# Kernel optimization log

Measured on AMD Instinct MI355X. Metric: run time of the kernel, lower is better.

## Reference

```python
import jax, jax.numpy as jnp
import numpy as np

B, N, K, G = 8, 2048, 20, 8
EPS = 1e-5

def lrelu(v):
    return jnp.where(v >= 0, v, 0.2 * v)

def group_norm(x, gamma, beta):
    # x: (B, C, ...); normalize over channel groups and spatial dims
    b, c = x.shape[0], x.shape[1]
    xg = x.reshape(b, G, c // G, -1)
    mu = xg.mean(axis=(2, 3), keepdims=True)
    var = xg.var(axis=(2, 3), keepdims=True)
    xn = ((xg - mu) * jax.lax.rsqrt(var + EPS)).reshape(x.shape)
    sh = (1, c) + (1,) * (x.ndim - 2)
    return xn * gamma.reshape(sh) + beta.reshape(sh)

def graph_feature(x, k):
    # x: (B, C, N) -> edge features (B, 2C, N, k)
    inner = 2.0 * jnp.einsum('bcn,bcm->bnm', x, x)
    xx = jnp.sum(x * x, axis=1)                     # (B, N)
    pd = -(xx[:, :, None] - inner + xx[:, None, :]) # negative squared dist
    idx = jax.lax.top_k(pd, k)[1]                   # (B, N, k) nearest
    xt = jnp.swapaxes(x, 1, 2)                      # (B, N, C)
    nbr = jax.vmap(lambda f, i: f[i])(xt, idx)      # (B, N, k, C) gather
    ctr = jnp.broadcast_to(xt[:, :, None, :], nbr.shape)
    feat = jnp.concatenate([nbr - ctr, ctr], axis=-1)  # (B, N, k, 2C)
    return jnp.transpose(feat, (0, 3, 1, 2))

def edge_block(x, w, b, g, h):
    f = graph_feature(x, K)
    y = jnp.einsum('oc,bcnk->bonk', w, f) + b[None, :, None, None]
    return lrelu(group_norm(y, g, h)).max(axis=-1)   # (B, out, N)

def _forward(x, w0, b0, g0, h0, w1, b1, g1, h1, w2, b2, g2, h2,
             w3, b3, g3, h3, fw0, fb0, fw1, fb1, fw2, fb2):
    cur = jnp.swapaxes(x, 1, 2)                      # (B, 3, N)
    res = []
    for (w, b, g, h) in ((w0, b0, g0, h0), (w1, b1, g1, h1), (w2, b2, g2, h2)):
        cur = edge_block(cur, w, b, g, h)
        res.append(cur)
    xc = jnp.concatenate(res, axis=1)                # (B, 256, N)
    pf = jnp.einsum('oc,bcn->bon', w3, xc) + b3[None, :, None]
    pf = lrelu(group_norm(pf, g3, h3))               # (B, 256, N)
    v = jnp.concatenate([pf.max(axis=-1), pf.mean(axis=-1)], axis=1)  # (B, 512)
    v = lrelu(v @ fw0.T + fb0)
    v = lrelu(v @ fw1.T + fb1)
    return v @ fw2.T + fb2                           # (B, 256)

def setup_inputs():
    key = jax.random.key(0)
    ks = jax.random.split(key, 16)
    def rn(k, shape, s=0.05):
        return jax.random.normal(k, shape, jnp.float32) * s
    inp = {'x': jax.random.normal(ks[0], (B, N, 3), jnp.float32)}
    inp.update(w0=rn(ks[1], (64, 6)), b0=rn(ks[2], (64,)), g0=jnp.ones((64,)), h0=jnp.zeros((64,)))
    inp.update(w1=rn(ks[3], (64, 128)), b1=rn(ks[4], (64,)), g1=jnp.ones((64,)), h1=jnp.zeros((64,)))
    inp.update(w2=rn(ks[5], (128, 128)), b2=rn(ks[6], (128,)), g2=jnp.ones((128,)), h2=jnp.zeros((128,)))
    inp.update(w3=rn(ks[7], (256, 256)), b3=rn(ks[8], (256,)), g3=jnp.ones((256,)), h3=jnp.zeros((256,)))
    inp.update(fw0=rn(ks[9], (512, 512)), fb0=rn(ks[10], (512,)))
    inp.update(fw1=rn(ks[11], (512, 512)), fb1=rn(ks[12], (512,)))
    inp.update(fw2=rn(ks[13], (256, 512)), fb2=rn(ks[14], (256,)))
    return inp

def reference(x, w0, b0, g0, h0, w1, b1, g1, h1, w2, b2, g2, h2,
              w3, b3, g3, h3, fw0, fb0, fw1, fb1, fw2, fb2):
    return _forward(x, w0, b0, g0, h0, w1, b1, g1, h1, w2, b2, g2, h2,
                    w3, b3, g3, h3, fw0, fb0, fw1, fb1, fw2, fb2)
```

## Files before the change

kernel.cpp:

```cpp
#include <hip/hip_runtime.h>
#include <hip/hip_bf16.h>
#include <cstdint>


constexpr int B = 8, N = 2048, KNN = 20, G = 8;
constexpr int BN = B * N;
constexpr float EPS = 1e-5f;

using bf16 = __hip_bfloat16;
using u64 = unsigned long long;

__device__ __forceinline__ float lrelu(float v){ return v >= 0.f ? v : 0.2f * v; }
__device__ __forceinline__ unsigned fenc(float f){ unsigned u = __float_as_uint(f); return (u & 0x80000000u) ? ~u : (u | 0x80000000u); }
__device__ __forceinline__ float fdec(unsigned u){ return (u & 0x80000000u) ? __uint_as_float(u & 0x7FFFFFFFu) : __uint_as_float(~u); }

template<int NB>
__device__ __forceinline__ void batcher_sort(unsigned* s){
  #pragma unroll
  for (int p = 1; p < NB; p <<= 1){
    #pragma unroll
    for (int k = p; k >= 1; k >>= 1){
      #pragma unroll
      for (int j = k % p; j <= NB-1-k; j += 2*k){
        #pragma unroll
        for (int i = 0; i <= ((k-1 < NB-1-j-k) ? k-1 : NB-1-j-k); ++i){
          if ((i + j) / (2*p) == (i + j + k) / (2*p)){
            const unsigned lo = min(s[i+j], s[i+j+k]);
            const unsigned hi = max(s[i+j], s[i+j+k]);
            s[i+j] = lo; s[i+j+k] = hi;
          }
        }
      }
    }
  }
}

template<int NB>
__device__ __forceinline__ void topk_update(unsigned* L, const unsigned* s){
  #pragma unroll
  for (int i = 0; i < NB; ++i) L[i] = min(L[i], s[i]);
  #pragma unroll
  for (int gap = 16; gap >= 1; gap >>= 1){
    #pragma unroll
    for (int i = 0; i < 32; ++i){
      if ((i & ((gap<<1)-1)) < gap){
        const unsigned hi = max(L[i], L[i+gap]);
        const unsigned lo = min(L[i], L[i+gap]);
        L[i] = hi; L[i+gap] = lo;
      }
    }
  }
}

__device__ __forceinline__ u64 knn_dec8(unsigned kk, int q){
  const unsigned ord = kk & 255u;
  const unsigned gidx = (ord >> 4)*128u + (unsigned)q + 8u*(ord & 15u);
  return ((u64)(kk & 0xFFFFFF00u) << 24) | gidx;
}

__device__ __forceinline__ void knn_merge32(unsigned char* ovl, const unsigned* L,
    int* __restrict__ knn_out, size_t bp, int r0, int sr, int sq){
  unsigned* mbuf = (unsigned*)ovl;
  #pragma unroll
  for (int k = 0; k < KNN; ++k) mbuf[(sr*8 + sq)*KNN + k] = L[31-k];
  __syncthreads();
  if (sq == 0){
    int h[8]; u64 v[8];
    #pragma unroll
    for (int q = 0; q < 8; ++q){ h[q] = 0; v[q] = knn_dec8(mbuf[(sr*8+q)*KNN], q); }
    int* outp = &knn_out[(bp + r0 + sr)*KNN];
    for (int k = 0; k < KNN; ++k){
      int best = 0; u64 bv = v[0];
      #pragma unroll
      for (int q = 1; q < 8; ++q) if (v[q] < bv){ bv = v[q]; best = q; }
      outp[k] = (int)(unsigned)(bv & 0xFFFFu);
      #pragma unroll
      for (int q = 0; q < 8; ++q) if (q == best){
        ++h[q];
        v[q] = (h[q] < KNN) ? knn_dec8(mbuf[(sr*8+q)*KNN + h[q]], q) : ~0ULL;
      }
    }
  }
}

struct SrcPtrs { const void* p[23]; };

__global__ __launch_bounds__(256) void convert_kernel(SrcPtrs sp, float* __restrict__ dst,
                                                      float* gstat, unsigned* vmax, float* vmean){
  if (blockIdx.y == 23){
    int t = blockIdx.x * 256 + threadIdx.x;
    if (t < 512) gstat[t] = 0.f;
    if (t < B*256){ vmax[t] = 0x007FFFFFu; vmean[t] = 0.f; }
    return;
  }
  constexpr int CNT[23] = {49152,384,64,64,64,8192,64,64,64,16384,128,128,128,
                           65536,256,256,256,262144,512,262144,512,131072,256};
  constexpr int OFF[23] = {0,49152,49536,49600,49664,49728,57920,57984,58048,58112,
                           74496,74624,74752,74880,140416,140672,140928,141184,
                           403328,403840,665984,666496,797568};
  const int ti = blockIdx.y;
  const int cnt = CNT[ti], off = OFF[ti];
  const unsigned g0w = *(const unsigned*)sp.p[3];
  const bool isbf = (g0w & 0xFFFFu) == 0x3F80u;
  const float* fs = (const float*)sp.p[ti];
  const unsigned short* bs = (const unsigned short*)sp.p[ti];
  for (int j = blockIdx.x*256 + threadIdx.x; j < cnt; j += gridDim.x*256){
    dst[off + j] = isbf ? __uint_as_float((unsigned)bs[j] << 16) : fs[j];
  }
}

template<int C>
__global__ __launch_bounds__(256) void sqnorm_cm(const float* __restrict__ f, float* __restrict__ cn){
  const int p = blockIdx.x*256 + threadIdx.x;
  float s = 0.f;
  #pragma unroll 8
  for (int c = 0; c < C; ++c){ const float v = f[(size_t)c*BN + p]; s += v*v; }
  cn[p] = s;
}

template<int C>
__global__ __launch_bounds__(256) void knn_kernel(const float* __restrict__ feat, const float* __restrict__ cnG,
                                                  int* __restrict__ knn_out){
  constexpr int ROWS = 32, CT = 128, DTP = 133;
  constexpr int COLF_BYTES = C*CT*4;
  __shared__ __align__(16) unsigned char ovl[COLF_BYTES];
  __shared__ __align__(16) float rowfT[C][ROWS];
  float* colfT = (float*)ovl;
  float* dbuf  = (float*)ovl;

  const int t = threadIdx.x;
  const int b = blockIdx.y;
  const int r0 = blockIdx.x * ROWS;
  const size_t bp = (size_t)b * N;
  const int rg = (t & 7)*4;
  const int cg = (t >> 3)*4;
  const int sr = t >> 3;
  const int sq = t & 7;
  const float rn = cnG[bp + r0 + sr];

  for (int i = t; i < C*(ROWS/4); i += 256){
    const int c = i >> 3, r4 = (i & 7)*4;
    *(float4*)&rowfT[c][r4] = *(const float4*)&feat[(size_t)c*BN + bp + r0 + r4];
  }

  unsigned L[32];
  #pragma unroll
  for (int k = 0; k < 32; ++k) L[k] = 0xFFFFFFFFu;

  for (int ct = 0; ct < N/CT; ++ct){
    const int m0 = ct * CT;
    __syncthreads();
    for (int i = t; i < C*(CT/4); i += 256){
      const int c = i >> 5, m4 = (i & 31)*4;
      *(float4*)&colfT[c*CT + m4] = *(const float4*)&feat[(size_t)c*BN + bp + m0 + m4];
    }
    const float4 cn4 = *(const float4*)&cnG[bp + m0 + cg];
    __syncthreads();

    float acc[4][4];
    #pragma unroll
    for (int i=0;i<4;i++){
      #pragma unroll
      for (int j=0;j<4;j++) acc[i][j]=0.f; }
    for (int c = 0; c < C; ++c){
      float4 ar = *(const float4*)&rowfT[c][rg];
      float4 cl = *(const float4*)&colfT[c*CT + cg];
      acc[0][0]+=ar.x*cl.x; acc[0][1]+=ar.x*cl.y; acc[0][2]+=ar.x*cl.z; acc[0][3]+=ar.x*cl.w;
      acc[1][0]+=ar.y*cl.x; acc[1][1]+=ar.y*cl.y; acc[1][2]+=ar.y*cl.z; acc[1][3]+=ar.y*cl.w;
      acc[2][0]+=ar.z*cl.x; acc[2][1]+=ar.z*cl.y; acc[2][2]+=ar.z*cl.z; acc[2][3]+=ar.z*cl.w;
      acc[3][0]+=ar.w*cl.x; acc[3][1]+=ar.w*cl.y; acc[3][2]+=ar.w*cl.z; acc[3][3]+=ar.w*cl.w;
    }
    __syncthreads();
    #pragma unroll
    for (int i=0;i<4;i++){
      float4 s;
      s.x = cn4.x - 2.f*acc[i][0]; s.y = cn4.y - 2.f*acc[i][1];
      s.z = cn4.z - 2.f*acc[i][2]; s.w = cn4.w - 2.f*acc[i][3];
      *(float4*)&dbuf[(rg+i)*DTP + cg] = s;
    }
    __syncthreads();

    const float* drow = &dbuf[sr*DTP];
    unsigned s16[16];
    #pragma unroll
    for (int j = 0; j < 16; ++j){
      const float d = fmaxf(drow[sq + 8*j] + rn, 0.f);
      s16[j] = (__float_as_uint(d) & 0xFFFFFF00u) | (unsigned)(ct*16 + j);
    }
    batcher_sort<16>(s16);
    topk_update<16>(L, s16);
  }

  __syncthreads();
  knn_merge32(ovl, L, knn_out, bp, r0, sr, sq);
}

__global__ __launch_bounds__(256) void knn3_kernel(const float* __restrict__ x, int* __restrict__ knn_out){
  constexpr int ROWS = 32, CT = 128;
  constexpr int MERGE_BYTES = ROWS*8*KNN*4;
  __shared__ __align__(16) unsigned char ovl[MERGE_BYTES];
  float* cx = (float*)ovl;
  float* cy = cx + CT;
  float* cz = cy + CT;

  const int t = threadIdx.x;
  const int b = blockIdx.y;
  const int r0 = blockIdx.x * ROWS;
  const size_t bp = (size_t)b * N;
  const int sr = t >> 3, sq = t & 7;
  const float rx = x[(bp + r0 + sr)*3 + 0];
  const float ry = x[(bp + r0 + sr)*3 + 1];
  const float rz = x[(bp + r0 + sr)*3 + 2];

  unsigned L[32];
  #pragma unroll
  for (int k = 0; k < 32; ++k) L[k] = 0xFFFFFFFFu;

  for (int ct = 0; ct < N/CT; ++ct){
    __syncthreads();
    if (t < CT){
      const size_t q = (bp + ct*CT + t)*3;
      cx[t] = x[q]; cy[t] = x[q+1]; cz[t] = x[q+2];
    }
    __syncthreads();
    unsigned s16[16];
    #pragma unroll
    for (int j = 0; j < 16; ++j){
      const int m = sq + 8*j;
      const float dx = rx - cx[m], dy = ry - cy[m], dz = rz - cz[m];
      const float d = dx*dx + dy*dy + dz*dz;
      s16[j] = (__float_as_uint(d) & 0xFFFFFF00u) | (unsigned)(ct*16 + j);
    }
    batcher_sort<16>(s16);
    topk_update<16>(L, s16);
  }

  __syncthreads();
  knn_merge32(ovl, L, knn_out, bp, r0, sr, sq);
}

template<int C, int COUT, int MT, bool CM>
__global__ __launch_bounds__(256) void zu_kernel(const float* __restrict__ feat, const float* __restrict__ w,
                                                 const float* __restrict__ bias,
                                                 float* __restrict__ z, float* __restrict__ u){
  __shared__ __align__(16) float fT[C][MT+4];
  __shared__ __align__(16) float Wt[C][COUT+4];
  const int t = threadIdx.x;
  const size_t p0 = (size_t)blockIdx.x * MT;
  if constexpr (CM){
    for (int i = t; i < C*(MT/4); i += 256){
      const int c = i / (MT/4), m4 = (i % (MT/4))*4;
      float4 v = *(const float4*)&feat[(size_t)c*BN + p0 + m4];
      *(float4*)&fT[c][m4] = v;
    }
  } else {
    for (int i = t; i < MT*C; i += 256){ int m = i / C, c = i - m*C; fT[c][m] = feat[(p0+m)*C + c]; }
  }
  for (int i = t; i < COUT*C; i += 256){ int o = i / C, c = i - o*C; Wt[c][o] = w[o*(2*C) + c]; }
  __syncthreads();
  constexpr int MQ = MT/4;
  const int rq = t % MQ, oq = t / MQ;
  const int mm = rq*4, oo = oq*8;
  float acc[4][8];
  #pragma unroll
  for (int i=0;i<4;i++){
    #pragma unroll
    for (int j=0;j<8;j++) acc[i][j] = 0.f; }
  for (int c = 0; c < C; ++c){
    float fr[4], wv[8];
    { float4 v = *(const float4*)&fT[c][mm]; fr[0]=v.x; fr[1]=v.y; fr[2]=v.z; fr[3]=v.w; }
    { float4 v = *(const float4*)&Wt[c][oo];   wv[0]=v.x; wv[1]=v.y; wv[2]=v.z; wv[3]=v.w; }
    { float4 v = *(const float4*)&Wt[c][oo+4]; wv[4]=v.x; wv[5]=v.y; wv[6]=v.z; wv[7]=v.w; }
    #pragma unroll
    for (int i=0;i<4;i++){
      #pragma unroll
      for (int j=0;j<8;j++) acc[i][j] += fr[i]*wv[j];
    }
  }
  #pragma unroll
  for (int i=0;i<4;i++){
    float4 s0, s1;
    s0.x=acc[i][0]; s0.y=acc[i][1]; s0.z=acc[i][2]; s0.w=acc[i][3];
    s1.x=acc[i][4]; s1.y=acc[i][5]; s1.z=acc[i][6]; s1.w=acc[i][7];
    *(float4*)&z[(p0+mm+i)*COUT + oo]     = s0;
    *(float4*)&z[(p0+mm+i)*COUT + oo + 4] = s1;
  }
  __syncthreads();
  for (int i = t; i < COUT*C; i += 256){
    int o = i / C, c = i - o*C;
    Wt[c][o] = w[o*2*C + C + c] - w[o*2*C + c];
  }
  __syncthreads();
  #pragma unroll
  for (int i=0;i<4;i++){
    #pragma unroll
    for (int j=0;j<8;j++) acc[i][j] = 0.f; }
  for (int c = 0; c < C; ++c){
    float fr[4], wv[8];
    { float4 v = *(const float4*)&fT[c][mm]; fr[0]=v.x; fr[1]=v.y; fr[2]=v.z; fr[3]=v.w; }
    { float4 v = *(const float4*)&Wt[c][oo];   wv[0]=v.x; wv[1]=v.y; wv[2]=v.z; wv[3]=v.w; }
    { float4 v = *(const float4*)&Wt[c][oo+4]; wv[4]=v.x; wv[5]=v.y; wv[6]=v.z; wv[7]=v.w; }
    #pragma unroll
    for (int i=0;i<4;i++){
      #pragma unroll
      for (int j=0;j<8;j++) acc[i][j] += fr[i]*wv[j];
    }
  }
  float bb[8];
  #pragma unroll
  for (int j=0;j<8;j++) bb[j] = bias[oo+j];
  #pragma unroll
  for (int i=0;i<4;i++){
    float4 s0, s1;
    s0.x=acc[i][0]+bb[0]; s0.y=acc[i][1]+bb[1]; s0.z=acc[i][2]+bb[2]; s0.w=acc[i][3]+bb[3];
    s1.x=acc[i][4]+bb[4]; s1.y=acc[i][5]+bb[5]; s1.z=acc[i][6]+bb[6]; s1.w=acc[i][7]+bb[7];
    *(float4*)&u[(p0+mm+i)*COUT + oo]     = s0;
    *(float4*)&u[(p0+mm+i)*COUT + oo + 4] = s1;
  }
}

template<int COUT, bool MM>
__global__ __launch_bounds__(256) void edge_stats_kernel(const float* __restrict__ z, const float* __restrict__ u,
                                                         const int* __restrict__ knn, float* __restrict__ gstat,
                                                         float* __restrict__ emax, float* __restrict__ emin){
  constexpr int REPS = 256 / COUT;
  constexpr int PPT  = 16 / REPS;
  __shared__ float red[G*2];
  const int t = threadIdx.x;
  const int o = t % COUT, pr = t / COUT;
  const size_t base = (size_t)blockIdx.x * 16;
  const int b = (int)(base / N);
  if (t < G*2) red[t] = 0.f;
  __syncthreads();
  float s1 = 0.f, s2 = 0.f;
  for (int j = 0; j < PPT; ++j){
    const size_t p = base + pr + (size_t)j*REPS;
    const float uu = u[p*COUT + o];
    const int* kn = knn + p*KNN;
    float mx = -3.0e38f, mn = 3.0e38f;
    for (int k = 0; k < KNN; ++k){
      const int m = kn[k];
      const float y = z[((size_t)b*N + m)*COUT + o] + uu;
      s1 += y; s2 += y*y;
      mx = fmaxf(mx, y); mn = fminf(mn, y);
    }
    if constexpr (MM){
      emax[p*COUT + o] = mx;
      emin[p*COUT + o] = mn;
    }
  }
  const int g = o / (COUT/G);
  atomicAdd(&red[g*2+0], s1);
  atomicAdd(&red[g*2+1], s2);
  __syncthreads();
  if (t < G*2) atomicAdd(&gstat[b*(G*2) + t], red[t]);
}

__global__ __launch_bounds__(256) void edge_norm_t64(const float* __restrict__ emax, const float* __restrict__ emin,
    const float* __restrict__ gstat, const float* __restrict__ gamma, const float* __restrict__ beta,
    float* __restrict__ fout, float cntInv){
  __shared__ float tile[64][68];
  const int t = threadIdx.x;
  const size_t p0 = (size_t)blockIdx.x * 64;
  const int b = (int)(p0 / N);
  const int o4 = (t & 15) * 4;
  float sc[4], sh[4];
  #pragma unroll
  for (int e = 0; e < 4; ++e){
    const int o = o4 + e;
    const int g = o >> 3;
    const float s1 = gstat[b*16 + g*2+0], s2 = gstat[b*16 + g*2+1];
    const float mu = s1*cntInv, var = s2*cntInv - mu*mu;
    const float inv = rsqrtf(var + EPS);
    sc[e] = gamma[o]*inv; sh[e] = beta[o] - mu*sc[e];
  }
  #pragma unroll
  for (int j = 0; j < 4; ++j){
    const int p = (t >> 4) + 16*j;
    float4 mx = *(const float4*)&emax[(p0+p)*64 + o4];
    float4 mn = *(const float4*)&emin[(p0+p)*64 + o4];
    float4 r;
    r.x = lrelu(sc[0]*(sc[0]>=0.f?mx.x:mn.x)+sh[0]);
    r.y = lrelu(sc[1]*(sc[1]>=0.f?mx.y:mn.y)+sh[1]);
    r.z = lrelu(sc[2]*(sc[2]>=0.f?mx.z:mn.z)+sh[2]);
    r.w = lrelu(sc[3]*(sc[3]>=0.f?mx.w:mn.w)+sh[3]);
    *(float4*)&tile[p][o4] = r;
  }
  __syncthreads();
  const int o = t >> 2;
  #pragma unroll
  for (int jj = 0; jj < 4; ++jj){
    const int p = (t & 3)*4 + 16*jj;
    float4 r;
    r.x = tile[p+0][o]; r.y = tile[p+1][o]; r.z = tile[p+2][o]; r.w = tile[p+3][o];
    *(float4*)&fout[(size_t)o*BN + p0 + p] = r;
  }
}

template<int COUT>
__global__ __launch_bounds__(256) void edge_norm_rm(const float* __restrict__ emax, const float* __restrict__ emin,
    const float* __restrict__ gstat, const float* __restrict__ gamma, const float* __restrict__ beta,
    float* __restrict__ fout, float cntInv){
  const size_t base = ((size_t)blockIdx.x*256 + threadIdx.x)*4;
  const int o = (int)(base & (COUT-1));
  const int b = (int)(base / ((size_t)N*COUT));
  const int g = o / (COUT/G);
  const float s1 = gstat[b*(G*2) + g*2 + 0];
  const float s2 = gstat[b*(G*2) + g*2 + 1];
  const float mu  = s1 * cntInv;
  const float var = s2 * cntInv - mu*mu;
  const float inv = rsqrtf(var + EPS);
  float4 gm = *(const float4*)&gamma[o];
  float4 bt = *(const float4*)&beta[o];
  float4 mx = *(const float4*)&emax[base];
  float4 mn = *(const float4*)&emin[base];
  float4 r;
  { const float sc = gm.x*inv, sh = bt.x - mu*sc; r.x = lrelu(sc*(sc>=0.f?mx.x:mn.x)+sh); }
  { const float sc = gm.y*inv, sh = bt.y - mu*sc; r.y = lrelu(sc*(sc>=0.f?mx.y:mn.y)+sh); }
  { const float sc = gm.z*inv, sh = bt.z - mu*sc; r.z = lrelu(sc*(sc>=0.f?mx.z:mn.z)+sh); }
  { const float sc = gm.w*inv, sh = bt.w - mu*sc; r.w = lrelu(sc*(sc>=0.f?mx.w:mn.w)+sh); }
  *(float4*)&fout[base] = r;
}

template<int COUT>
__global__ __launch_bounds__(256) void edge_norm_kernel(const float* __restrict__ z, const float* __restrict__ u,
    const int* __restrict__ knn, const float* __restrict__ gstat,
    const float* __restrict__ gamma, const float* __restrict__ beta,
    float* __restrict__ fout, float cntInv){
  constexpr int REPS = 256 / COUT;
  constexpr int PPT  = 16 / REPS;
  const int t = threadIdx.x;
  const int o = t % COUT, pr = t / COUT;
  const size_t base = (size_t)blockIdx.x * 16;
  const int b = (int)(base / N);
  const int g = o / (COUT/G);
  const float s1 = gstat[b*(G*2) + g*2 + 0];
  const float s2 = gstat[b*(G*2) + g*2 + 1];
  const float mu  = s1 * cntInv;
  const float var = s2 * cntInv - mu*mu;
  const float inv = rsqrtf(var + EPS);
  const float sc = gamma[o] * inv;
  const float sh = beta[o] - mu * sc;
  for (int j = 0; j < PPT; ++j){
    const size_t p = base + pr + (size_t)j*REPS;
    const float uu = u[p*COUT + o];
    const int* kn = knn + p*KNN;
    float mx = -3.0e38f;
    for (int k = 0; k < KNN; ++k){
      const int m = kn[k];
      const float y = z[((size_t)b*N + m)*COUT + o] + uu;
      mx = fmaxf(mx, lrelu(sc*y + sh));
    }
    fout[p*COUT + o] = mx;
  }
}

__global__ __launch_bounds__(256) void conv3_kernel(const float* __restrict__ f1, const float* __restrict__ f2,
    const float* __restrict__ f3, const float* __restrict__ w3, const float* __restrict__ b3,
    float* __restrict__ y3, float* __restrict__ gstat){
  __shared__ __align__(16) float fT[32][64+4];
  __shared__ __align__(16) float Wt[32][256+4];
  __shared__ float red[G*2];
  const int t = threadIdx.x;
  const size_t p0 = (size_t)blockIdx.x * 64;
  const int b = (int)(p0 / N);
  const int rq = t & 15, oq = t >> 4;
  const int mm = rq*4, oo = oq*16;
  if (t < G*2) red[t] = 0.f;
  float acc[4][16];
  #pragma unroll
  for (int i=0;i<4;i++){
    #pragma unroll
    for (int j=0;j<16;j++) acc[i][j] = 0.f; }
  for (int cc = 0; cc < 8; ++cc){
    __syncthreads();
    if (cc < 4){
      const float* src = (cc < 2) ? f1 : f2;
      const int coff = (cc & 1)*32;
      for (int i = t; i < 512; i += 256){
        const int c = i >> 4, m4 = (i & 15)*4;
        float4 v = *(const float4*)&src[(size_t)(coff+c)*BN + p0 + m4];
        *(float4*)&fT[c][m4] = v;
      }
    } else {
      const int coff = (cc-4)*32;
      for (int i = t; i < 512; i += 256){
        const int m = i >> 3, cq = (i & 7)*4;
        float4 v = *(const float4*)&f3[(p0+m)*128 + coff + cq];
        fT[cq+0][m]=v.x; fT[cq+1][m]=v.y; fT[cq+2][m]=v.z; fT[cq+3][m]=v.w;
      }
    }
    for (int i = t; i < 2048; i += 256){
      int o = i >> 3, cq = (i & 7)*4;
      float4 v = *(const float4*)&w3[(size_t)o*256 + cc*32 + cq];
      Wt[cq+0][o]=v.x; Wt[cq+1][o]=v.y; Wt[cq+2][o]=v.z; Wt[cq+3][o]=v.w;
    }
    __syncthreads();
    for (int c = 0; c < 32; ++c){
      float fr[4], wv[16];
      { float4 v = *(const float4*)&fT[c][mm]; fr[0]=v.x; fr[1]=v.y; fr[2]=v.z; fr[3]=v.w; }
      { float4 v = *(const float4*)&Wt[c][oo+0];  wv[0]=v.x;  wv[1]=v.y;  wv[2]=v.z;  wv[3]=v.w;  }
      { float4 v = *(const float4*)&Wt[c][oo+4];  wv[4]=v.x;  wv[5]=v.y;  wv[6]=v.z;  wv[7]=v.w;  }
      { float4 v = *(const float4*)&Wt[c][oo+8];  wv[8]=v.x;  wv[9]=v.y;  wv[10]=v.z; wv[11]=v.w; }
      { float4 v = *(const float4*)&Wt[c][oo+12]; wv[12]=v.x; wv[13]=v.y; wv[14]=v.z; wv[15]=v.w; }
      #pragma unroll
      for (int i=0;i<4;i++){
        #pragma unroll
        for (int j=0;j<16;j++) acc[i][j] += fr[i]*wv[j];
      }
    }
  }
  float bb[16];
  #pragma unroll
  for (int j=0;j<16;j++) bb[j] = b3[oo+j];
  float s1 = 0.f, s2 = 0.f;
  #pragma unroll
  for (int i=0;i<4;i++){
    #pragma unroll
    for (int j=0;j<16;j++){
      acc[i][j] += bb[j];
      s1 += acc[i][j]; s2 += acc[i][j]*acc[i][j];
    }
  }
  #pragma unroll
  for (int i=0;i<4;i++){
    #pragma unroll
    for (int q=0;q<4;q++){
      float4 s;
      s.x=acc[i][q*4+0]; s.y=acc[i][q*4+1]; s.z=acc[i][q*4+2]; s.w=acc[i][q*4+3];
      *(float4*)&y3[(p0+mm+i)*256 + oo + q*4] = s;
    }
  }
  const int g = oo >> 5;
  atomicAdd(&red[g*2+0], s1);
  atomicAdd(&red[g*2+1], s2);
  __syncthreads();
  if (t < G*2) atomicAdd(&gstat[b*(G*2) + t], red[t]);
}

__global__ __launch_bounds__(256) void pf_kernel(const float* __restrict__ y3, const float* __restrict__ gstat,
    const float* __restrict__ g3, const float* __restrict__ h3,
    unsigned* __restrict__ vmax, float* __restrict__ vmean){
  const int o = threadIdx.x;
  const int b = blockIdx.y;
  const int n0 = blockIdx.x * 64;
  const int g = o >> 5;
  const float cntInv = 1.f/(32.f*N);
  const float s1 = gstat[b*(G*2)+g*2+0], s2 = gstat[b*(G*2)+g*2+1];
  const float mu = s1*cntInv, var = s2*cntInv - mu*mu;
  const float inv = rsqrtf(var + EPS);
  const float sc = g3[o] * inv;
  const float sh = h3[o] - mu*sc;
  float mx = -3.0e38f, sm = 0.f;
  for (int n = n0; n < n0+64; ++n){
    float v = y3[((size_t)b*N + n)*256 + o];
    v = lrelu(sc*v + sh);
    mx = fmaxf(mx, v);
    sm += v;
  }
  atomicMax(&vmax[b*256+o], fenc(mx));
  atomicAdd(&vmean[b*256+o], sm * (1.f/N));
}

__global__ __launch_bounds__(256) void fc_fused(const unsigned* __restrict__ vmax, const float* __restrict__ vmean,
    const float* __restrict__ fw0, const float* __restrict__ fb0,
    const float* __restrict__ fw1, const float* __restrict__ fb1,
    const float* __restrict__ fw2, const float* __restrict__ fb2,
    void* outp, const unsigned* __restrict__ dflag){
  __shared__ float va[512], vb[512];
  const int t = threadIdx.x, b = blockIdx.x;
  for (int c = t; c < 512; c += 256)
    va[c] = (c < 256) ? fdec(vmax[b*256 + c]) : vmean[b*256 + (c-256)];
  __syncthreads();
  {
    float a0 = fb0[t], a1 = fb0[t+256];
    const float* w0p = fw0 + (size_t)t*512;
    const float* w1p = fw0 + (size_t)(t+256)*512;
    for (int c = 0; c < 512; c += 4){
      float4 wa = *(const float4*)&w0p[c];
      float4 wb = *(const float4*)&w1p[c];
      a0 += wa.x*va[c+0] + wa.y*va[c+1] + wa.z*va[c+2] + wa.w*va[c+3];
      a1 += wb.x*va[c+0] + wb.y*va[c+1] + wb.z*va[c+2] + wb.w*va[c+3];
    }
    vb[t] = lrelu(a0); vb[t+256] = lrelu(a1);
  }
  __syncthreads();
  {
    float a0 = fb1[t], a1 = fb1[t+256];
    const float* w0p = fw1 + (size_t)t*512;
    const float* w1p = fw1 + (size_t)(t+256)*512;
    for (int c = 0; c < 512; c += 4){
      float4 wa = *(const float4*)&w0p[c];
      float4 wb = *(const float4*)&w1p[c];
      a0 += wa.x*vb[c+0] + wa.y*vb[c+1] + wa.z*vb[c+2] + wa.w*vb[c+3];
      a1 += wb.x*vb[c+0] + wb.y*vb[c+1] + wb.z*vb[c+2] + wb.w*vb[c+3];
    }
    va[t] = lrelu(a0); va[t+256] = lrelu(a1);
  }
  __syncthreads();
  {
    float a = fb2[t];
    const float* wp = fw2 + (size_t)t*512;
    for (int c = 0; c < 512; c += 4){
      float4 wv = *(const float4*)&wp[c];
      a += wv.x*va[c+0] + wv.y*va[c+1] + wv.z*va[c+2] + wv.w*va[c+3];
    }
    const bool isbf = ((*dflag) & 0xFFFFu) == 0x3F80u;
    if (isbf) ((bf16*)outp)[b*256 + t] = __float2bfloat16(a);
    else      ((float*)outp)[b*256 + t] = a;
  }
}

extern "C" void kernel_launch(void* const* d_in, const int* in_sizes, int n_in,
                              void* d_out, int out_size, void* d_ws, size_t ws_size,
                              hipStream_t stream){
  (void)in_sizes; (void)n_in; (void)out_size;

  float* ws = (float*)d_ws;
  float* f1 = ws;
  float* f2 = f1 + (size_t)64*BN;
  float* f3 = f2 + (size_t)64*BN;
  float* zb = f3 + (size_t)128*BN;
  float* ub = zb + (size_t)128*BN;
  int*   kn = (int*)(ub + (size_t)128*BN);
  float* gs = (float*)(kn + (size_t)BN*KNN);
  unsigned* vmax = (unsigned*)(gs + 512);
  float* vmean = (float*)(vmax + B*256);
  float* cnG = vmean + B*256;
  float* pc = cnG + (size_t)BN;
  float* y3 = zb;
  float* emax2 = pc + 797824;
  float* emin2 = emax2 + (size_t)128*BN;
  const size_t need2 = (size_t)((emin2 + (size_t)128*BN) - ws) * 4;
  const bool fused2 = (ws_size >= need2);
  float* emax01 = f3;
  float* emin01 = f3 + (size_t)64*BN;

  const float* xc  = pc + 0;
  const float* w0c = pc + 49152;  const float* b0c = pc + 49536;
  const float* g0c = pc + 49600;  const float* h0c = pc + 49664;
  const float* w1c = pc + 49728;  const float* b1c = pc + 57920;
  const float* g1c = pc + 57984;  const float* h1c = pc + 58048;
  const float* w2c = pc + 58112;  const float* b2c = pc + 74496;
  const float* g2c = pc + 74624;  const float* h2c = pc + 74752;
  const float* w3c = pc + 74880;  const float* b3c = pc + 140416;
  const float* g3c = pc + 140672; const float* h3c = pc + 140928;
  const float* fw0c= pc + 141184; const float* fb0c= pc + 403328;
  const float* fw1c= pc + 403840; const float* fb1c= pc + 665984;
  const float* fw2c= pc + 666496; const float* fb2c= pc + 797568;

  SrcPtrs sp;
  for (int i = 0; i < 23; ++i) sp.p[i] = d_in[i];
  convert_kernel<<<dim3(64, 24), 256, 0, stream>>>(sp, pc, gs, vmax, vmean);

  knn3_kernel<<<dim3(N/32, B), 256, 0, stream>>>(xc, kn);
  zu_kernel<3, 64, 128, false><<<BN/128, 256, 0, stream>>>(xc, w0c, b0c, zb, ub);
  edge_stats_kernel<64,true><<<BN/16, 256, 0, stream>>>(zb, ub, kn, gs + 0, emax01, emin01);
  edge_norm_t64<<<BN/64, 256, 0, stream>>>(emax01, emin01, gs + 0, g0c, h0c, f1, 1.f/327680.f);

  sqnorm_cm<64><<<BN/256, 256, 0, stream>>>(f1, cnG);
  knn_kernel<64><<<dim3(N/32, B), 256, 0, stream>>>(f1, cnG, kn);
  zu_kernel<64, 64, 128, true><<<BN/128, 256, 0, stream>>>(f1, w1c, b1c, zb, ub);
  edge_stats_kernel<64,true><<<BN/16, 256, 0, stream>>>(zb, ub, kn, gs + 128, emax01, emin01);
  edge_norm_t64<<<BN/64, 256, 0, stream>>>(emax01, emin01, gs + 128, g1c, h1c, f2, 1.f/327680.f);

  sqnorm_cm<64><<<BN/256, 256, 0, stream>>>(f2, cnG);
  knn_kernel<64><<<dim3(N/32, B), 256, 0, stream>>>(f2, cnG, kn);
  zu_kernel<64, 128, 64, true><<<BN/64, 256, 0, stream>>>(f2, w2c, b2c, zb, ub);
  if (fused2){
    edge_stats_kernel<128,true><<<BN/16, 256, 0, stream>>>(zb, ub, kn, gs + 256, emax2, emin2);
    edge_norm_rm<128><<<(BN*128)/1024, 256, 0, stream>>>(emax2, emin2, gs + 256, g2c, h2c, f3, 1.f/655360.f);
  } else {
    edge_stats_kernel<128,false><<<BN/16, 256, 0, stream>>>(zb, ub, kn, gs + 256, nullptr, nullptr);
    edge_norm_kernel<128><<<BN/16, 256, 0, stream>>>(zb, ub, kn, gs + 256, g2c, h2c, f3, 1.f/655360.f);
  }

  conv3_kernel<<<BN/64, 256, 0, stream>>>(f1, f2, f3, w3c, b3c, y3, gs + 384);
  pf_kernel<<<dim3(32, B), 256, 0, stream>>>(y3, gs + 384, g3c, h3c, vmax, vmean);

  fc_fused<<<B, 256, 0, stream>>>(vmax, vmean, fw0c, fb0c, fw1c, fb1c, fw2c, fb2c,
                                  d_out, (const unsigned*)d_in[3]);
}
```

Baseline: 679.5 us.

## Split KNN column range across two blocks and merge partial top-k lists

Each KNN kernel now launches a z-dimension of two, with each block scanning half of the candidate columns and writing a sorted 64-bit (distance, index) top-20 list to a scratch buffer aliased on ub. A new knn_fin kernel merges the two partial lists per point into the final index array. The aim is to double the number of blocks (512 to 1024) for better occupancy of the GPU's compute units. In exchange it adds extra launches and extra global traffic for the partial lists, plus duplicated row loads and merge work per half.

```diff
diff --git a/kernel.cpp b/kernel.cpp
--- a/kernel.cpp
+++ b/kernel.cpp
@@ -52,14 +52,14 @@
   }
 }
 
-__device__ __forceinline__ u64 knn_dec8(unsigned kk, int q){
+__device__ __forceinline__ u64 knn_dec8(unsigned kk, int q, int half){
   const unsigned ord = kk & 255u;
-  const unsigned gidx = (ord >> 4)*128u + (unsigned)q + 8u*(ord & 15u);
+  const unsigned gidx = (unsigned)(half*8 + (ord >> 4))*128u + (unsigned)q + 8u*(ord & 15u);
   return ((u64)(kk & 0xFFFFFF00u) << 24) | gidx;
 }
 
-__device__ __forceinline__ void knn_merge32(unsigned char* ovl, const unsigned* L,
-    int* __restrict__ knn_out, size_t bp, int r0, int sr, int sq){
+__device__ __forceinline__ void knn_merge_out(unsigned char* ovl, const unsigned* L,
+    u64* __restrict__ kn2, size_t bp, int r0, int sr, int sq, int half){
   unsigned* mbuf = (unsigned*)ovl;
   #pragma unroll
   for (int k = 0; k < KNN; ++k) mbuf[(sr*8 + sq)*KNN + k] = L[31-k];
@@ -67,19 +67,32 @@
   if (sq == 0){
     int h[8]; u64 v[8];
     #pragma unroll
-    for (int q = 0; q < 8; ++q){ h[q] = 0; v[q] = knn_dec8(mbuf[(sr*8+q)*KNN], q); }
-    int* outp = &knn_out[(bp + r0 + sr)*KNN];
+    for (int q = 0; q < 8; ++q){ h[q] = 0; v[q] = knn_dec8(mbuf[(sr*8+q)*KNN], q, half); }
+    u64* outp = &kn2[((bp + r0 + sr)*2 + half)*KNN];
     for (int k = 0; k < KNN; ++k){
       int best = 0; u64 bv = v[0];
       #pragma unroll
       for (int q = 1; q < 8; ++q) if (v[q] < bv){ bv = v[q]; best = q; }
-      outp[k] = (int)(unsigned)(bv & 0xFFFFu);
+      outp[k] = bv;
       #pragma unroll
       for (int q = 0; q < 8; ++q) if (q == best){
         ++h[q];
-        v[q] = (h[q] < KNN) ? knn_dec8(mbuf[(sr*8+q)*KNN + h[q]], q) : ~0ULL;
+        v[q] = (h[q] < KNN) ? knn_dec8(mbuf[(sr*8+q)*KNN + h[q]], q, half) : ~0ULL;
       }
     }
+  }
+}
+
+__global__ __launch_bounds__(256) void knn_fin(const u64* __restrict__ kn2, int* __restrict__ kn){
+  const int p = blockIdx.x*256 + threadIdx.x;
+  const u64* la = &kn2[(size_t)p*2*KNN];
+  const u64* lb = la + KNN;
+  int* outp = &kn[(size_t)p*KNN];
+  int ia = 0, ib = 0;
+  for (int k = 0; k < KNN; ++k){
+    const u64 a = la[ia], c = lb[ib];
+    if (a <= c){ outp[k] = (int)(unsigned)(a & 0xFFFFu); ++ia; }
+    else       { outp[k] = (int)(unsigned)(c & 0xFFFFu); ++ib; }
   }
 }
 
@@ -120,7 +133,7 @@
 
 template<int C>
 __global__ __launch_bounds__(256) void knn_kernel(const float* __restrict__ feat, const float* __restrict__ cnG,
-                                                  int* __restrict__ knn_out){
+                                                  u64* __restrict__ kn2){
   constexpr int ROWS = 32, CT = 128, DTP = 133;
   constexpr int COLF_BYTES = C*CT*4;
   __shared__ __align__(16) unsigned char ovl[COLF_BYTES];
@@ -130,6 +143,7 @@
 
   const int t = threadIdx.x;
   const int b = blockIdx.y;
+  const int half = blockIdx.z;
   const int r0 = blockIdx.x * ROWS;
   const size_t bp = (size_t)b * N;
   const int rg = (t & 7)*4;
@@ -147,8 +161,8 @@
   #pragma unroll
   for (int k = 0; k < 32; ++k) L[k] = 0xFFFFFFFFu;
 
-  for (int ct = 0; ct < N/CT; ++ct){
-    const int m0 = ct * CT;
+  for (int ct = 0; ct < 8; ++ct){
+    const int m0 = (half*8 + ct) * CT;
     __syncthreads();
     for (int i = t; i < C*(CT/4); i += 256){
       const int c = i >> 5, m4 = (i & 31)*4;
@@ -192,10 +206,10 @@
   }
 
   __syncthreads();
-  knn_merge32(ovl, L, knn_out, bp, r0, sr, sq);
-}
-
-__global__ __launch_bounds__(256) void knn3_kernel(const float* __restrict__ x, int* __restrict__ knn_out){
+  knn_merge_out(ovl, L, kn2, bp, r0, sr, sq, half);
+}
+
+__global__ __launch_bounds__(256) void knn3_kernel(const float* __restrict__ x, u64* __restrict__ kn2){
   constexpr int ROWS = 32, CT = 128;
   constexpr int MERGE_BYTES = ROWS*8*KNN*4;
   __shared__ __align__(16) unsigned char ovl[MERGE_BYTES];
@@ -205,6 +219,7 @@
 
   const int t = threadIdx.x;
   const int b = blockIdx.y;
+  const int half = blockIdx.z;
   const int r0 = blockIdx.x * ROWS;
   const size_t bp = (size_t)b * N;
   const int sr = t >> 3, sq = t & 7;
@@ -216,10 +231,10 @@
   #pragma unroll
   for (int k = 0; k < 32; ++k) L[k] = 0xFFFFFFFFu;
 
-  for (int ct = 0; ct < N/CT; ++ct){
+  for (int ct = 0; ct < 8; ++ct){
     __syncthreads();
     if (t < CT){
-      const size_t q = (bp + ct*CT + t)*3;
+      const size_t q = (bp + (half*8 + ct)*CT + t)*3;
       cx[t] = x[q]; cy[t] = x[q+1]; cz[t] = x[q+2];
     }
     __syncthreads();
@@ -236,7 +251,7 @@
   }
 
   __syncthreads();
-  knn_merge32(ovl, L, knn_out, bp, r0, sr, sq);
+  knn_merge_out(ovl, L, kn2, bp, r0, sr, sq, half);
 }
 
 template<int C, int COUT, int MT, bool CM>
@@ -629,6 +644,7 @@
   float* cnG = vmean + B*256;
   float* pc = cnG + (size_t)BN;
   float* y3 = zb;
+  u64* kn2 = (u64*)ub;
   float* emax2 = pc + 797824;
   float* emin2 = emax2 + (size_t)128*BN;
   const size_t need2 = (size_t)((emin2 + (size_t)128*BN) - ws) * 4;
@@ -653,19 +669,22 @@
   for (int i = 0; i < 23; ++i) sp.p[i] = d_in[i];
   convert_kernel<<<dim3(64, 24), 256, 0, stream>>>(sp, pc, gs, vmax, vmean);
 
-  knn3_kernel<<<dim3(N/32, B), 256, 0, stream>>>(xc, kn);
+  knn3_kernel<<<dim3(N/32, B, 2), 256, 0, stream>>>(xc, kn2);
+  knn_fin<<<BN/256, 256, 0, stream>>>(kn2, kn);
   zu_kernel<3, 64, 128, false><<<BN/128, 256, 0, stream>>>(xc, w0c, b0c, zb, ub);
   edge_stats_kernel<64,true><<<BN/16, 256, 0, stream>>>(zb, ub, kn, gs + 0, emax01, emin01);
   edge_norm_t64<<<BN/64, 256, 0, stream>>>(emax01, emin01, gs + 0, g0c, h0c, f1, 1.f/327680.f);
 
   sqnorm_cm<64><<<BN/256, 256, 0, stream>>>(f1, cnG);
-  knn_kernel<64><<<dim3(N/32, B), 256, 0, stream>>>(f1, cnG, kn);
+  knn_kernel<64><<<dim3(N/32, B, 2), 256, 0, stream>>>(f1, cnG, kn2);
+  knn_fin<<<BN/256, 256, 0, stream>>>(kn2, kn);
   zu_kernel<64, 64, 128, true><<<BN/128, 256, 0, stream>>>(f1, w1c, b1c, zb, ub);
   edge_stats_kernel<64,true><<<BN/16, 256, 0, stream>>>(zb, ub, kn, gs + 128, emax01, emin01);
   edge_norm_t64<<<BN/64, 256, 0, stream>>>(emax01, emin01, gs + 128, g1c, h1c, f2, 1.f/327680.f);
 
   sqnorm_cm<64><<<BN/256, 256, 0, stream>>>(f2, cnG);
-  knn_kernel<64><<<dim3(N/32, B), 256, 0, stream>>>(f2, cnG, kn);
+  knn_kernel<64><<<dim3(N/32, B, 2), 256, 0, stream>>>(f2, cnG, kn2);
+  knn_fin<<<BN/256, 256, 0, stream>>>(kn2, kn);
   zu_kernel<64, 128, 64, true><<<BN/64, 256, 0, stream>>>(f2, w2c, b2c, zb, ub);
   if (fused2){
     edge_stats_kernel<128,true><<<BN/16, 256, 0, stream>>>(zb, ub, kn, gs + 256, emax2, emin2);
```

Measured after the change: 686.8 us. Within noise of the previous version (+1.1%).
